# Optimization experiments

Measured on AMD Instinct MI355X. Metric: run time of the kernel, lower is better.

Reference implementation:

```python
import jax, jax.numpy as jnp
import numpy as np

B, K, D = 16384, 32, 64
N_USERS, N_ENT, N_REL = 100000, 100000, 32
MAX_NORM = 1.0


def renorm(e):
    # emulate torch nn.Embedding(max_norm=1): rescale rows with norm > 1
    n = jnp.linalg.norm(e, axis=-1, keepdims=True)
    return e * jnp.minimum(1.0, MAX_NORM / jnp.maximum(n, 1e-7))


def setup_inputs() -> dict:
    key = jax.random.key(0)
    ks = jax.random.split(key, 9)
    return {
        "user_table": jax.random.normal(ks[0], (N_USERS, D), dtype=jnp.float32),
        "entity_table": jax.random.normal(ks[1], (N_ENT, D), dtype=jnp.float32),
        "relation_table": jax.random.normal(ks[2], (N_REL, D), dtype=jnp.float32),
        "W": jax.random.normal(ks[3], (D, D), dtype=jnp.float32) / np.sqrt(D),
        "b": jnp.zeros((D,), dtype=jnp.float32),
        "users": jax.random.randint(ks[4], (B,), 0, N_USERS),
        "items": jax.random.randint(ks[5], (B,), 0, N_ENT),
        "adj_entity": jax.random.randint(ks[6], (N_ENT, K), 0, N_ENT),
        "adj_relation": jax.random.randint(ks[7], (N_ENT, K), 0, N_REL),
    }


def reference(user_table, entity_table, relation_table, W, b,
              users, items, adj_entity, adj_relation):
    # neighbor id gather: [B, K]
    nbr_ent_ids = adj_entity[items]
    nbr_rel_ids = adj_relation[items]
    # embedding lookups with max_norm renorm
    user_emb = renorm(user_table[users])                 # [B, D]
    item_emb = renorm(entity_table[items])               # [B, D]
    nbr_ent = renorm(entity_table[nbr_ent_ids])          # [B, K, D]
    nbr_rel = renorm(relation_table[nbr_rel_ids])        # [B, K, D]
    # user-relation attention scores, softmax over neighbors
    scores = jnp.einsum('bd,bkd->bk', user_emb, nbr_rel)  # [B, K]
    attn = jax.nn.softmax(scores, axis=-1)
    # attention-weighted neighbor aggregation
    nbr_vec = jnp.einsum('bk,bkd->bd', attn, nbr_ent)     # [B, D]
    # sum aggregator + linear + relu (dropout omitted: eval-mode baseline)
    out = item_emb + nbr_vec
    out = jax.nn.relu(out @ W.T + b)
    return (user_emb, out)
```

## Files before the change

### kernel.cpp

```cpp
#include <hip/hip_runtime.h>
#include <math.h>

#define BB 16384
#define KK_N 32
#define DD 64
#define N_ENT 100000
#define N_REL 32
#define NBLK 4096

__device__ __forceinline__ float dot4(float4 a, float4 b) {
    return a.x * b.x + a.y * b.y + a.z * b.z + a.w * b.w;
}

__global__ __launch_bounds__(256) void kgcn_fused(
    const float* __restrict__ user_table,
    const float* __restrict__ entity_table,
    const float* __restrict__ relation_table,
    const float* __restrict__ W,
    const float* __restrict__ bias,
    const int*   __restrict__ users,
    const int*   __restrict__ items,
    const int*   __restrict__ adj_entity,
    const int*   __restrict__ adj_relation,
    float* __restrict__ out_user,
    float* __restrict__ out_final)
{
    __shared__ __align__(16) float Wlds[64 * 64];
    __shared__ __align__(16) float RelLds[N_REL * DD];
    __shared__ __align__(16) float Vec[4][64];

    const int tid  = threadIdx.x;
    const int lane = tid & 63;
    const int wave = tid >> 6;
    const int grp  = lane >> 4;
    const int gl   = lane & 15;

    const int b = blockIdx.x * 4 + wave;
    const int uid = __builtin_amdgcn_readfirstlane(users[b]);
    const int iid = __builtin_amdgcn_readfirstlane(items[b]);

    const int kk = lane & 31;
    const int* abase = (lane < 32) ? adj_entity : adj_relation;
    const int adjv = abase[(size_t)iid * KK_N + kk];
    float4 uv = *reinterpret_cast<const float4*>(&user_table[(size_t)uid * DD + gl * 4]);
    float4 iv = *reinterpret_cast<const float4*>(&entity_table[(size_t)iid * DD + gl * 4]);

    #pragma unroll
    for (int it = 0; it < 4; ++it) {
        int i = tid + it * 256;
        float4 w4 = reinterpret_cast<const float4*>(W)[i];
        int d = i >> 4;
        int j = (i & 15) * 4;
        *reinterpret_cast<float4*>(&Wlds[d * 64 + (j ^ ((d & 15) << 2))]) = w4;
    }
    #pragma unroll
    for (int it = 0; it < 2; ++it) {
        int r = wave * 8 + it * 4 + grp;
        float4 v = reinterpret_cast<const float4*>(relation_table)[r * 16 + gl];
        float ss = dot4(v, v);
        #pragma unroll
        for (int m = 1; m < 16; m <<= 1) ss += __shfl_xor(ss, m, 64);
        float sc = fminf(1.0f, __builtin_amdgcn_rsqf(ss));
        v.x *= sc; v.y *= sc; v.z *= sc; v.w *= sc;
        *reinterpret_cast<float4*>(&RelLds[r * 64 + ((gl * 4) ^ ((r & 15) << 2))]) = v;
    }

    float ssu = dot4(uv, uv);
    #pragma unroll
    for (int m = 1; m < 16; m <<= 1) ssu += __shfl_xor(ssu, m, 64);
    float usc = fminf(1.0f, __builtin_amdgcn_rsqf(ssu));
    uv.x *= usc; uv.y *= usc; uv.z *= usc; uv.w *= usc;
    if (lane < 16)
        *reinterpret_cast<float4*>(&out_user[(size_t)b * DD + gl * 4]) = uv;

    int   eid[8];
    #pragma unroll
    for (int k0 = 0; k0 < 8; ++k0)
        eid[k0] = __shfl(adjv, k0 * 4 + grp, 64);
    float4 v[8];
    #pragma unroll
    for (int k0 = 0; k0 < 8; ++k0)
        v[k0] = *reinterpret_cast<const float4*>(&entity_table[(size_t)eid[k0] * DD + gl * 4]);

    __syncthreads();
    if (lane < 16)
        *reinterpret_cast<float4*>(&Vec[wave][gl * 4]) = uv;

    const int rid = __shfl(adjv, 32 + kk, 64);
    const int srel = (rid & 15) << 2;
    const float* relrow = &RelLds[rid * 64];
    const int dbase = (lane >> 5) * 32;
    float score = 0.0f;
    #pragma unroll
    for (int d0 = 0; d0 < 32; d0 += 4) {
        int d = dbase + d0;
        float4 rv = *reinterpret_cast<const float4*>(&relrow[d ^ srel]);
        float4 tv = *reinterpret_cast<const float4*>(&Vec[wave][d]);
        score += dot4(tv, rv);
    }
    score += __shfl_xor(score, 32, 64);

    float mx = score;
    #pragma unroll
    for (int m = 1; m < 32; m <<= 1) mx = fmaxf(mx, __shfl_xor(mx, m, 64));
    float e = __expf(score - mx);
    float sum = e;
    #pragma unroll
    for (int m = 1; m < 32; m <<= 1) sum += __shfl_xor(sum, m, 64);
    const float attn = e * __builtin_amdgcn_rcpf(sum);

    float cc[8];
    #pragma unroll
    for (int k0 = 0; k0 < 8; ++k0)
        cc[k0] = __shfl(attn, k0 * 4 + grp, 64);

    float4 acc = make_float4(0.f, 0.f, 0.f, 0.f);
    #pragma unroll
    for (int k0 = 0; k0 < 8; ++k0) {
        float ss = dot4(v[k0], v[k0]);
        #pragma unroll
        for (int m = 1; m < 16; m <<= 1) ss += __shfl_xor(ss, m, 64);
        float sc = fminf(1.0f, __builtin_amdgcn_rsqf(ss));
        float ck = cc[k0] * sc;
        acc.x = fmaf(ck, v[k0].x, acc.x);
        acc.y = fmaf(ck, v[k0].y, acc.y);
        acc.z = fmaf(ck, v[k0].z, acc.z);
        acc.w = fmaf(ck, v[k0].w, acc.w);
    }
    #pragma unroll
    for (int m = 16; m < 64; m <<= 1) {
        acc.x += __shfl_xor(acc.x, m, 64);
        acc.y += __shfl_xor(acc.y, m, 64);
        acc.z += __shfl_xor(acc.z, m, 64);
        acc.w += __shfl_xor(acc.w, m, 64);
    }

    float ssi = dot4(iv, iv);
    #pragma unroll
    for (int m = 1; m < 16; m <<= 1) ssi += __shfl_xor(ssi, m, 64);
    float isc = fminf(1.0f, __builtin_amdgcn_rsqf(ssi));
    float4 tmp;
    tmp.x = fmaf(isc, iv.x, acc.x);
    tmp.y = fmaf(isc, iv.y, acc.y);
    tmp.z = fmaf(isc, iv.z, acc.z);
    tmp.w = fmaf(isc, iv.w, acc.w);
    if (lane < 16)
        *reinterpret_cast<float4*>(&Vec[wave][gl * 4]) = tmp;

    const float bv = bias[lane];
    const float* wrow = &Wlds[lane * 64];
    const int twz = (lane & 15) << 2;
    float o = bv;
    #pragma unroll
    for (int j0 = 0; j0 < 64; j0 += 4) {
        float4 wv = *reinterpret_cast<const float4*>(&wrow[j0 ^ twz]);
        float4 tv = *reinterpret_cast<const float4*>(&Vec[wave][j0]);
        o += dot4(tv, wv);
    }
    out_final[(size_t)b * DD + lane] = fmaxf(o, 0.0f);
}

extern "C" void kernel_launch(void* const* d_in, const int* in_sizes, int n_in,
                              void* d_out, int out_size, void* d_ws, size_t ws_size,
                              hipStream_t stream)
{
    const float* user_table     = (const float*)d_in[0];
    const float* entity_table   = (const float*)d_in[1];
    const float* relation_table = (const float*)d_in[2];
    const float* W              = (const float*)d_in[3];
    const float* bias           = (const float*)d_in[4];
    const int*   users          = (const int*)d_in[5];
    const int*   items          = (const int*)d_in[6];
    const int*   adj_entity     = (const int*)d_in[7];
    const int*   adj_relation   = (const int*)d_in[8];

    float* out_user  = (float*)d_out;
    float* out_final = (float*)d_out + (size_t)BB * DD;

    kgcn_fused<<<NBLK, 256, 0, stream>>>(user_table, entity_table, relation_table,
                                         W, bias, users, items, adj_entity, adj_relation,
                                         out_user, out_final);
}
```

Baseline: 31.38 us.

## Precompute per-entity renorm scales in a separate pass before main kernel

Adds a precompute kernel that computes the max-norm scale for every entity row, writes the renormalized user rows straight to the output, and stores renormalized relation rows in workspace. The main kernel then reads these scales instead of redoing the per-neighbour norm reductions and shuffles, and loads the relation table from workspace. It also moves to 512-thread blocks handling 8 batch rows each. The cost is a full extra pass over the entity table plus a second kernel launch, which may outweigh the arithmetic and shuffle work removed from the gather-bound main kernel.

```diff
diff --git a/kernel.cpp b/kernel.cpp
--- a/kernel.cpp
+++ b/kernel.cpp
@@ -6,87 +6,117 @@
 #define DD 64
 #define N_ENT 100000
 #define N_REL 32
-#define NBLK 4096
+
+
+#define T_ENT  N_ENT
+#define T_USER (N_ENT + BB)
+#define T_ALL  (N_ENT + BB + N_REL)
 
 __device__ __forceinline__ float dot4(float4 a, float4 b) {
     return a.x * b.x + a.y * b.y + a.z * b.z + a.w * b.w;
 }
 
-__global__ __launch_bounds__(256) void kgcn_fused(
+__device__ __forceinline__ float red16(float ss) {
+    ss += __shfl_xor(ss, 1, 64);
+    ss += __shfl_xor(ss, 2, 64);
+    ss += __shfl_xor(ss, 4, 64);
+    ss += __shfl_xor(ss, 8, 64);
+    return ss;
+}
+
+__global__ __launch_bounds__(256) void precompute(
     const float* __restrict__ user_table,
     const float* __restrict__ entity_table,
     const float* __restrict__ relation_table,
+    const int*   __restrict__ users,
+    float* __restrict__ ws,
+    float* __restrict__ out_user)
+{
+    const int tid = threadIdx.x;
+    const int gl  = tid & 15;
+    const int t   = blockIdx.x * 16 + (tid >> 4);
+
+    if (t < T_ENT) {
+        float4 v = *reinterpret_cast<const float4*>(&entity_table[(size_t)t * DD + gl * 4]);
+        float ss = red16(dot4(v, v));
+        float sc = fminf(1.0f, __builtin_amdgcn_rsqf(ss));
+        if (gl == 0) ws[t] = sc;
+    } else if (t < T_USER) {
+        int u = t - T_ENT;
+        int uid = users[u];
+        float4 v = *reinterpret_cast<const float4*>(&user_table[(size_t)uid * DD + gl * 4]);
+        float ss = red16(dot4(v, v));
+        float sc = fminf(1.0f, __builtin_amdgcn_rsqf(ss));
+        v.x *= sc; v.y *= sc; v.z *= sc; v.w *= sc;
+        *reinterpret_cast<float4*>(&out_user[(size_t)u * DD + gl * 4]) = v;
+    } else if (t < T_ALL) {
+        int r = t - T_USER;
+        float4 v = *reinterpret_cast<const float4*>(&relation_table[r * DD + gl * 4]);
+        float ss = red16(dot4(v, v));
+        float sc = fminf(1.0f, __builtin_amdgcn_rsqf(ss));
+        v.x *= sc; v.y *= sc; v.z *= sc; v.w *= sc;
+        *reinterpret_cast<float4*>(&ws[N_ENT + r * 64 + ((gl * 4) ^ ((r & 15) << 2))]) = v;
+    }
+}
+
+__global__ __launch_bounds__(512, 8) void kgcn_main(
+    const float* __restrict__ entity_table,
+    const float* __restrict__ ws,
     const float* __restrict__ W,
     const float* __restrict__ bias,
-    const int*   __restrict__ users,
     const int*   __restrict__ items,
     const int*   __restrict__ adj_entity,
     const int*   __restrict__ adj_relation,
-    float* __restrict__ out_user,
+    const float* __restrict__ user_out,
     float* __restrict__ out_final)
 {
     __shared__ __align__(16) float Wlds[64 * 64];
     __shared__ __align__(16) float RelLds[N_REL * DD];
-    __shared__ __align__(16) float Vec[4][64];
+    __shared__ __align__(16) float Vec[8][64];
 
     const int tid  = threadIdx.x;
     const int lane = tid & 63;
     const int wave = tid >> 6;
     const int grp  = lane >> 4;
     const int gl   = lane & 15;
-
-    const int b = blockIdx.x * 4 + wave;
-    const int uid = __builtin_amdgcn_readfirstlane(users[b]);
+    const int kk   = lane & 31;
+
+    const int b = blockIdx.x * 8 + wave;
     const int iid = __builtin_amdgcn_readfirstlane(items[b]);
 
-    const int kk = lane & 31;
     const int* abase = (lane < 32) ? adj_entity : adj_relation;
     const int adjv = abase[(size_t)iid * KK_N + kk];
-    float4 uv = *reinterpret_cast<const float4*>(&user_table[(size_t)uid * DD + gl * 4]);
+    const float sg = ws[adjv];
+    const float isc = ws[iid];
+    float4 uv = *reinterpret_cast<const float4*>(&user_out[(size_t)b * DD + gl * 4]);
     float4 iv = *reinterpret_cast<const float4*>(&entity_table[(size_t)iid * DD + gl * 4]);
-
-    #pragma unroll
-    for (int it = 0; it < 4; ++it) {
-        int i = tid + it * 256;
+    const float bv = bias[lane];
+
+    int eid[8];
+    #pragma unroll
+    for (int k0 = 0; k0 < 8; ++k0)
+        eid[k0] = __shfl(adjv, k0 * 4 + grp, 64);
+    float4 v[8];
+    #pragma unroll
+    for (int k0 = 0; k0 < 8; ++k0)
+        v[k0] = *reinterpret_cast<const float4*>(&entity_table[(size_t)eid[k0] * DD + gl * 4]);
+
+    #pragma unroll
+    for (int it = 0; it < 2; ++it) {
+        int i = tid + it * 512;
         float4 w4 = reinterpret_cast<const float4*>(W)[i];
         int d = i >> 4;
         int j = (i & 15) * 4;
         *reinterpret_cast<float4*>(&Wlds[d * 64 + (j ^ ((d & 15) << 2))]) = w4;
     }
-    #pragma unroll
-    for (int it = 0; it < 2; ++it) {
-        int r = wave * 8 + it * 4 + grp;
-        float4 v = reinterpret_cast<const float4*>(relation_table)[r * 16 + gl];
-        float ss = dot4(v, v);
-        #pragma unroll
-        for (int m = 1; m < 16; m <<= 1) ss += __shfl_xor(ss, m, 64);
-        float sc = fminf(1.0f, __builtin_amdgcn_rsqf(ss));
-        v.x *= sc; v.y *= sc; v.z *= sc; v.w *= sc;
-        *reinterpret_cast<float4*>(&RelLds[r * 64 + ((gl * 4) ^ ((r & 15) << 2))]) = v;
-    }
-
-    float ssu = dot4(uv, uv);
-    #pragma unroll
-    for (int m = 1; m < 16; m <<= 1) ssu += __shfl_xor(ssu, m, 64);
-    float usc = fminf(1.0f, __builtin_amdgcn_rsqf(ssu));
-    uv.x *= usc; uv.y *= usc; uv.z *= usc; uv.w *= usc;
-    if (lane < 16)
-        *reinterpret_cast<float4*>(&out_user[(size_t)b * DD + gl * 4]) = uv;
-
-    int   eid[8];
-    #pragma unroll
-    for (int k0 = 0; k0 < 8; ++k0)
-        eid[k0] = __shfl(adjv, k0 * 4 + grp, 64);
-    float4 v[8];
-    #pragma unroll
-    for (int k0 = 0; k0 < 8; ++k0)
-        v[k0] = *reinterpret_cast<const float4*>(&entity_table[(size_t)eid[k0] * DD + gl * 4]);
+    reinterpret_cast<float4*>(RelLds)[tid] = reinterpret_cast<const float4*>(ws + N_ENT)[tid];
 
     __syncthreads();
+
     if (lane < 16)
         *reinterpret_cast<float4*>(&Vec[wave][gl * 4]) = uv;
 
-    const int rid = __shfl(adjv, 32 + kk, 64);
+    const int rid  = __shfl(adjv, 32 + kk, 64);
     const int srel = (rid & 15) << 2;
     const float* relrow = &RelLds[rid * 64];
     const int dbase = (lane >> 5) * 32;
@@ -107,21 +137,12 @@
     float sum = e;
     #pragma unroll
     for (int m = 1; m < 32; m <<= 1) sum += __shfl_xor(sum, m, 64);
-    const float attn = e * __builtin_amdgcn_rcpf(sum);
-
-    float cc[8];
-    #pragma unroll
-    for (int k0 = 0; k0 < 8; ++k0)
-        cc[k0] = __shfl(attn, k0 * 4 + grp, 64);
+    const float wk = e * __builtin_amdgcn_rcpf(sum) * sg;
 
     float4 acc = make_float4(0.f, 0.f, 0.f, 0.f);
     #pragma unroll
     for (int k0 = 0; k0 < 8; ++k0) {
-        float ss = dot4(v[k0], v[k0]);
-        #pragma unroll
-        for (int m = 1; m < 16; m <<= 1) ss += __shfl_xor(ss, m, 64);
-        float sc = fminf(1.0f, __builtin_amdgcn_rsqf(ss));
-        float ck = cc[k0] * sc;
+        float ck = __shfl(wk, k0 * 4 + grp, 64);
         acc.x = fmaf(ck, v[k0].x, acc.x);
         acc.y = fmaf(ck, v[k0].y, acc.y);
         acc.z = fmaf(ck, v[k0].z, acc.z);
@@ -135,10 +156,6 @@
         acc.w += __shfl_xor(acc.w, m, 64);
     }
 
-    float ssi = dot4(iv, iv);
-    #pragma unroll
-    for (int m = 1; m < 16; m <<= 1) ssi += __shfl_xor(ssi, m, 64);
-    float isc = fminf(1.0f, __builtin_amdgcn_rsqf(ssi));
     float4 tmp;
     tmp.x = fmaf(isc, iv.x, acc.x);
     tmp.y = fmaf(isc, iv.y, acc.y);
@@ -147,7 +164,6 @@
     if (lane < 16)
         *reinterpret_cast<float4*>(&Vec[wave][gl * 4]) = tmp;
 
-    const float bv = bias[lane];
     const float* wrow = &Wlds[lane * 64];
     const int twz = (lane & 15) << 2;
     float o = bv;
@@ -174,10 +190,13 @@
     const int*   adj_entity     = (const int*)d_in[7];
     const int*   adj_relation   = (const int*)d_in[8];
 
+    float* ws        = (float*)d_ws;
     float* out_user  = (float*)d_out;
     float* out_final = (float*)d_out + (size_t)BB * DD;
 
-    kgcn_fused<<<NBLK, 256, 0, stream>>>(user_table, entity_table, relation_table,
-                                         W, bias, users, items, adj_entity, adj_relation,
-                                         out_user, out_final);
-}
+    precompute<<<(T_ALL + 15) / 16, 256, 0, stream>>>(user_table, entity_table, relation_table,
+                                                      users, ws, out_user);
+    kgcn_main<<<BB / 8, 512, 0, stream>>>(entity_table, ws, W, bias,
+                                          items, adj_entity, adj_relation,
+                                          out_user, out_final);
+}
```

New measurement: 56.46 us. 79.9% more time.

## Precompute renormalized entity-times-W table and split into precompute and main kernels

Applied to the files above, without the earlier changes.

Because the final linear layer is linear, W is applied to every renormalized entity row in a precompute kernel, written to workspace. The main kernel then only gathers the transformed rows, mixes them with attention weights, adds bias and applies ReLU, with no per-sample 64x64 matvec. The precompute kernel also writes the renormalized user rows and a swizzled renormalized relation table. The softmax max-subtraction is dropped because all scores have magnitude at most 1 after renormalization. This trades per-sample W work and repeated renorms for a full pass over all 100k entities each call, plus the workspace write and a second launch.

```diff
diff --git a/kernel.cpp b/kernel.cpp
--- a/kernel.cpp
+++ b/kernel.cpp
@@ -6,10 +6,181 @@
 #define DD 64
 #define N_ENT 100000
 #define N_REL 32
-#define NBLK 4096
+
+#define NB_EW ((N_ENT + 63) / 64)
+#define NB_U  (BB / 16)
+#define NB_R  2
+#define GRID_PRE (NB_EW + NB_U + NB_R)
+
+#define WS_REL_OFF ((size_t)N_ENT * DD)
+#define WS_NEED_BYTES ((WS_REL_OFF + (size_t)N_REL * DD) * 4)
 
 __device__ __forceinline__ float dot4(float4 a, float4 b) {
     return a.x * b.x + a.y * b.y + a.z * b.z + a.w * b.w;
+}
+
+__device__ __forceinline__ float red16(float ss) {
+    ss += __shfl_xor(ss, 1, 64);
+    ss += __shfl_xor(ss, 2, 64);
+    ss += __shfl_xor(ss, 4, 64);
+    ss += __shfl_xor(ss, 8, 64);
+    return ss;
+}
+
+__global__ __launch_bounds__(256) void precompute(
+    const float* __restrict__ user_table,
+    const float* __restrict__ entity_table,
+    const float* __restrict__ relation_table,
+    const float* __restrict__ W,
+    const int*   __restrict__ users,
+    float* __restrict__ ws,
+    float* __restrict__ out_user)
+{
+    const int tid = threadIdx.x;
+    const int blk = blockIdx.x;
+
+    if (blk < NB_EW) {
+        const int lane = tid & 63;
+        const int row  = blk * 64 + lane;
+        const int d0   = __builtin_amdgcn_readfirstlane(tid >> 6) * 16;
+        const int r    = (row < N_ENT) ? row : 0;
+        const float* arow = entity_table + (size_t)r * DD;
+
+        float acc[16];
+        #pragma unroll
+        for (int i = 0; i < 16; ++i) acc[i] = 0.0f;
+        float ss = 0.0f;
+
+        #pragma unroll 1
+        for (int j0 = 0; j0 < DD; j0 += 4) {
+            float4 a = *reinterpret_cast<const float4*>(&arow[j0]);
+            ss += dot4(a, a);
+            #pragma unroll
+            for (int dd = 0; dd < 16; ++dd) {
+                float4 w = *reinterpret_cast<const float4*>(&W[(d0 + dd) * DD + j0]);
+                acc[dd] = fmaf(a.x, w.x, fmaf(a.y, w.y, fmaf(a.z, w.z, fmaf(a.w, w.w, acc[dd]))));
+            }
+        }
+        float sc = fminf(1.0f, __builtin_amdgcn_rsqf(ss));
+        if (row < N_ENT) {
+            #pragma unroll
+            for (int q = 0; q < 4; ++q) {
+                float4 o = make_float4(acc[q*4+0]*sc, acc[q*4+1]*sc, acc[q*4+2]*sc, acc[q*4+3]*sc);
+                *reinterpret_cast<float4*>(&ws[(size_t)row * DD + d0 + q * 4]) = o;
+            }
+        }
+    } else if (blk < NB_EW + NB_U) {
+        const int gl = tid & 15;
+        const int u  = (blk - NB_EW) * 16 + (tid >> 4);
+        const int uid = users[u];
+        float4 v = *reinterpret_cast<const float4*>(&user_table[(size_t)uid * DD + gl * 4]);
+        float ss = red16(dot4(v, v));
+        float sc = fminf(1.0f, __builtin_amdgcn_rsqf(ss));
+        v.x *= sc; v.y *= sc; v.z *= sc; v.w *= sc;
+        *reinterpret_cast<float4*>(&out_user[(size_t)u * DD + gl * 4]) = v;
+    } else {
+        const int gl = tid & 15;
+        const int rr = (blk - NB_EW - NB_U) * 16 + (tid >> 4);
+        float4 v = *reinterpret_cast<const float4*>(&relation_table[rr * DD + gl * 4]);
+        float ss = red16(dot4(v, v));
+        float sc = fminf(1.0f, __builtin_amdgcn_rsqf(ss));
+        v.x *= sc; v.y *= sc; v.z *= sc; v.w *= sc;
+        *reinterpret_cast<float4*>(&ws[WS_REL_OFF + rr * DD + ((gl * 4) ^ ((rr & 15) << 2))]) = v;
+    }
+}
+
+__global__ __launch_bounds__(256) void kgcn_main(
+    const float* __restrict__ ew,
+    const float* __restrict__ rel_ws,
+    const float* __restrict__ bias,
+    const int*   __restrict__ items,
+    const int*   __restrict__ adj_entity,
+    const int*   __restrict__ adj_relation,
+    const float* __restrict__ user_out,
+    float* __restrict__ out_final)
+{
+    __shared__ __align__(16) float RelLds[N_REL * DD];
+    __shared__ __align__(16) float Vec[4][64];
+
+    const int tid  = threadIdx.x;
+    const int lane = tid & 63;
+    const int wave = tid >> 6;
+    const int grp  = lane >> 4;
+    const int gl   = lane & 15;
+    const int kk   = lane & 31;
+
+    const int b = blockIdx.x * 4 + wave;
+    const int iid = __builtin_amdgcn_readfirstlane(items[b]);
+
+    const int* abase = (lane < 32) ? adj_entity : adj_relation;
+    const int adjv = abase[(size_t)iid * KK_N + kk];
+    float4 uv    = *reinterpret_cast<const float4*>(&user_out[(size_t)b * DD + gl * 4]);
+    float4 ewi   = *reinterpret_cast<const float4*>(&ew[(size_t)iid * DD + gl * 4]);
+    float4 bias4 = *reinterpret_cast<const float4*>(&bias[gl * 4]);
+
+    int eid[8];
+    #pragma unroll
+    for (int k0 = 0; k0 < 8; ++k0)
+        eid[k0] = adj_entity[(size_t)iid * KK_N + k0 * 4 + grp];
+    float4 v[8];
+    #pragma unroll
+    for (int k0 = 0; k0 < 8; ++k0)
+        v[k0] = *reinterpret_cast<const float4*>(&ew[(size_t)eid[k0] * DD + gl * 4]);
+
+    #pragma unroll
+    for (int it = 0; it < 2; ++it)
+        reinterpret_cast<float4*>(RelLds)[tid + it * 256] =
+            reinterpret_cast<const float4*>(rel_ws)[tid + it * 256];
+    __syncthreads();
+
+    if (lane < 16)
+        *reinterpret_cast<float4*>(&Vec[wave][gl * 4]) = uv;
+
+    const int rid  = __shfl(adjv, 32 + kk, 64);
+    const int srel = (rid & 15) << 2;
+    const float* relrow = &RelLds[rid * DD];
+    const int dbase = (lane >> 5) * 32;
+    float score = 0.0f;
+    #pragma unroll
+    for (int d0 = 0; d0 < 32; d0 += 4) {
+        int d = dbase + d0;
+        float4 rv = *reinterpret_cast<const float4*>(&relrow[d ^ srel]);
+        float4 tv = *reinterpret_cast<const float4*>(&Vec[wave][d]);
+        score += dot4(tv, rv);
+    }
+    score += __shfl_xor(score, 32, 64);
+
+    float e = __expf(score);
+    float sum = e;
+    #pragma unroll
+    for (int m = 1; m < 32; m <<= 1) sum += __shfl_xor(sum, m, 64);
+    const float wk = e * __builtin_amdgcn_rcpf(sum);
+
+    float4 acc = make_float4(0.f, 0.f, 0.f, 0.f);
+    #pragma unroll
+    for (int k0 = 0; k0 < 8; ++k0) {
+        float ck = __shfl(wk, k0 * 4 + grp, 64);
+        acc.x = fmaf(ck, v[k0].x, acc.x);
+        acc.y = fmaf(ck, v[k0].y, acc.y);
+        acc.z = fmaf(ck, v[k0].z, acc.z);
+        acc.w = fmaf(ck, v[k0].w, acc.w);
+    }
+    #pragma unroll
+    for (int m = 16; m < 64; m <<= 1) {
+        acc.x += __shfl_xor(acc.x, m, 64);
+        acc.y += __shfl_xor(acc.y, m, 64);
+        acc.z += __shfl_xor(acc.z, m, 64);
+        acc.w += __shfl_xor(acc.w, m, 64);
+    }
+
+    if (lane < 16) {
+        float4 o;
+        o.x = fmaxf(ewi.x + acc.x + bias4.x, 0.0f);
+        o.y = fmaxf(ewi.y + acc.y + bias4.y, 0.0f);
+        o.z = fmaxf(ewi.z + acc.z + bias4.z, 0.0f);
+        o.w = fmaxf(ewi.w + acc.w + bias4.w, 0.0f);
+        *reinterpret_cast<float4*>(&out_final[(size_t)b * DD + gl * 4]) = o;
+    }
 }
 
 __global__ __launch_bounds__(256) void kgcn_fused(
@@ -56,13 +227,13 @@
     #pragma unroll
     for (int it = 0; it < 2; ++it) {
         int r = wave * 8 + it * 4 + grp;
-        float4 v = reinterpret_cast<const float4*>(relation_table)[r * 16 + gl];
-        float ss = dot4(v, v);
+        float4 vv = reinterpret_cast<const float4*>(relation_table)[r * 16 + gl];
+        float ss = dot4(vv, vv);
         #pragma unroll
         for (int m = 1; m < 16; m <<= 1) ss += __shfl_xor(ss, m, 64);
         float sc = fminf(1.0f, __builtin_amdgcn_rsqf(ss));
-        v.x *= sc; v.y *= sc; v.z *= sc; v.w *= sc;
-        *reinterpret_cast<float4*>(&RelLds[r * 64 + ((gl * 4) ^ ((r & 15) << 2))]) = v;
+        vv.x *= sc; vv.y *= sc; vv.z *= sc; vv.w *= sc;
+        *reinterpret_cast<float4*>(&RelLds[r * 64 + ((gl * 4) ^ ((r & 15) << 2))]) = vv;
     }
 
     float ssu = dot4(uv, uv);
@@ -73,7 +244,7 @@
     if (lane < 16)
         *reinterpret_cast<float4*>(&out_user[(size_t)b * DD + gl * 4]) = uv;
 
-    int   eid[8];
+    int eid[8];
     #pragma unroll
     for (int k0 = 0; k0 < 8; ++k0)
         eid[k0] = __shfl(adjv, k0 * 4 + grp, 64);
@@ -174,10 +345,19 @@
     const int*   adj_entity     = (const int*)d_in[7];
     const int*   adj_relation   = (const int*)d_in[8];
 
+    float* ws        = (float*)d_ws;
     float* out_user  = (float*)d_out;
     float* out_final = (float*)d_out + (size_t)BB * DD;
 
-    kgcn_fused<<<NBLK, 256, 0, stream>>>(user_table, entity_table, relation_table,
-                                         W, bias, users, items, adj_entity, adj_relation,
-                                         out_user, out_final);
-}
+    if (ws_size >= WS_NEED_BYTES) {
+        precompute<<<GRID_PRE, 256, 0, stream>>>(user_table, entity_table, relation_table,
+                                                 W, users, ws, out_user);
+        kgcn_main<<<BB / 4, 256, 0, stream>>>(ws, ws + WS_REL_OFF, bias,
+                                              items, adj_entity, adj_relation,
+                                              out_user, out_final);
+    } else {
+        kgcn_fused<<<BB / 4, 256, 0, stream>>>(user_table, entity_table, relation_table,
+                                               W, bias, users, items, adj_entity, adj_relation,
+                                               out_user, out_final);
+    }
+}
```

Measured after the change: 51.70 us. 1.65x slower.

## Pre-renormalize entity table to bf16 in a workspace pass before main kernel

Applied to the files above, without the earlier changes.

A new precompute kernel renormalizes the whole entity table once per call and stores it as bf16 in the workspace. The same pass writes the renormalized user rows and a swizzled relation table. The main kernel then gathers half-width neighbor rows with no per-neighbor norm work, handles two batch rows per wave, and drops the softmax max subtraction because scores are bounded once rows are renormalized. This trades an extra full-table pass and a second launch for less gather traffic and ALU work, at the cost of bf16 rounding in the entity embeddings.

```diff
diff --git a/kernel.cpp b/kernel.cpp
--- a/kernel.cpp
+++ b/kernel.cpp
@@ -6,10 +6,226 @@
 #define DD 64
 #define N_ENT 100000
 #define N_REL 32
-#define NBLK 4096
+
+#define WS_REL_OFF_BYTES ((size_t)N_ENT * DD * 2)
+#define WS_NEED_BYTES (WS_REL_OFF_BYTES + (size_t)N_REL * DD * 4)
+
+#define PT_ENT  N_ENT
+#define PT_USER (N_ENT + BB)
+#define PT_ALL  (N_ENT + BB + N_REL)
 
 __device__ __forceinline__ float dot4(float4 a, float4 b) {
     return a.x * b.x + a.y * b.y + a.z * b.z + a.w * b.w;
+}
+
+__device__ __forceinline__ float red16(float ss) {
+    ss += __shfl_xor(ss, 1, 64);
+    ss += __shfl_xor(ss, 2, 64);
+    ss += __shfl_xor(ss, 4, 64);
+    ss += __shfl_xor(ss, 8, 64);
+    return ss;
+}
+
+__device__ __forceinline__ unsigned short f2bf(float x) {
+    unsigned int u = __float_as_uint(x);
+    u += 0x7fffu + ((u >> 16) & 1u);
+    return (unsigned short)(u >> 16);
+}
+
+__device__ __forceinline__ float bf2f(unsigned short h) {
+    return __uint_as_float(((unsigned int)h) << 16);
+}
+
+__device__ __forceinline__ float4 bf4(ushort4 h) {
+    return make_float4(bf2f(h.x), bf2f(h.y), bf2f(h.z), bf2f(h.w));
+}
+
+__global__ __launch_bounds__(256) void precompute(
+    const float* __restrict__ user_table,
+    const float* __restrict__ entity_table,
+    const float* __restrict__ relation_table,
+    const int*   __restrict__ users,
+    unsigned short* __restrict__ ent_bf,
+    float* __restrict__ rel_ws,
+    float* __restrict__ out_user)
+{
+    const int tid = threadIdx.x;
+    const int gl  = tid & 15;
+    const int t   = blockIdx.x * 16 + (tid >> 4);
+    if (t >= PT_ALL) return;
+
+    if (t < PT_ENT) {
+        float4 v = *reinterpret_cast<const float4*>(&entity_table[(size_t)t * DD + gl * 4]);
+        float ss = red16(dot4(v, v));
+        float sc = fminf(1.0f, __builtin_amdgcn_rsqf(ss));
+        ushort4 h;
+        h.x = f2bf(v.x * sc); h.y = f2bf(v.y * sc);
+        h.z = f2bf(v.z * sc); h.w = f2bf(v.w * sc);
+        *reinterpret_cast<ushort4*>(&ent_bf[(size_t)t * DD + gl * 4]) = h;
+    } else if (t < PT_USER) {
+        int u = t - PT_ENT;
+        int uid = users[u];
+        float4 v = *reinterpret_cast<const float4*>(&user_table[(size_t)uid * DD + gl * 4]);
+        float ss = red16(dot4(v, v));
+        float sc = fminf(1.0f, __builtin_amdgcn_rsqf(ss));
+        v.x *= sc; v.y *= sc; v.z *= sc; v.w *= sc;
+        *reinterpret_cast<float4*>(&out_user[(size_t)u * DD + gl * 4]) = v;
+    } else {
+        int rr = t - PT_USER;
+        float4 v = *reinterpret_cast<const float4*>(&relation_table[rr * DD + gl * 4]);
+        float ss = red16(dot4(v, v));
+        float sc = fminf(1.0f, __builtin_amdgcn_rsqf(ss));
+        v.x *= sc; v.y *= sc; v.z *= sc; v.w *= sc;
+        *reinterpret_cast<float4*>(&rel_ws[rr * DD + ((gl * 4) ^ ((rr & 15) << 2))]) = v;
+    }
+}
+
+__global__ __launch_bounds__(256, 4) void kgcn_main(
+    const unsigned short* __restrict__ ent_bf,
+    const float* __restrict__ rel_ws,
+    const float* __restrict__ W,
+    const float* __restrict__ bias,
+    const int*   __restrict__ items,
+    const int*   __restrict__ adj_entity,
+    const int*   __restrict__ adj_relation,
+    const float* __restrict__ user_out,
+    float* __restrict__ out_final)
+{
+    __shared__ __align__(16) float Wlds[64 * 64];
+    __shared__ __align__(16) float RelLds[N_REL * DD];
+    __shared__ __align__(16) float Vec[4][2][64];
+
+    const int tid  = threadIdx.x;
+    const int lane = tid & 63;
+    const int wave = tid >> 6;
+    const int grp  = lane >> 4;
+    const int gl   = lane & 15;
+    const int kk   = lane & 31;
+
+    const int b0 = (blockIdx.x * 4 + wave) * 2;
+    const int iid0 = __builtin_amdgcn_readfirstlane(items[b0]);
+    const int iid1 = __builtin_amdgcn_readfirstlane(items[b0 + 1]);
+
+    const int* abase = (lane < 32) ? adj_entity : adj_relation;
+    const int adjv0 = abase[(size_t)iid0 * KK_N + kk];
+    const int adjv1 = abase[(size_t)iid1 * KK_N + kk];
+
+    int eid0[8], eid1[8];
+    #pragma unroll
+    for (int k0 = 0; k0 < 8; ++k0) {
+        eid0[k0] = adj_entity[(size_t)iid0 * KK_N + k0 * 4 + grp];
+        eid1[k0] = adj_entity[(size_t)iid1 * KK_N + k0 * 4 + grp];
+    }
+    ushort4 v0[8], v1[8];
+    #pragma unroll
+    for (int k0 = 0; k0 < 8; ++k0) {
+        v0[k0] = *reinterpret_cast<const ushort4*>(&ent_bf[(size_t)eid0[k0] * DD + gl * 4]);
+        v1[k0] = *reinterpret_cast<const ushort4*>(&ent_bf[(size_t)eid1[k0] * DD + gl * 4]);
+    }
+    float4 uv0 = *reinterpret_cast<const float4*>(&user_out[(size_t)b0 * DD + gl * 4]);
+    float4 uv1 = *reinterpret_cast<const float4*>(&user_out[(size_t)(b0 + 1) * DD + gl * 4]);
+    ushort4 it0 = *reinterpret_cast<const ushort4*>(&ent_bf[(size_t)iid0 * DD + gl * 4]);
+    ushort4 it1 = *reinterpret_cast<const ushort4*>(&ent_bf[(size_t)iid1 * DD + gl * 4]);
+
+    #pragma unroll
+    for (int it = 0; it < 4; ++it) {
+        int i = tid + it * 256;
+        float4 w4 = reinterpret_cast<const float4*>(W)[i];
+        int d = i >> 4;
+        int j = (i & 15) * 4;
+        *reinterpret_cast<float4*>(&Wlds[d * 64 + (j ^ ((d & 15) << 2))]) = w4;
+    }
+    #pragma unroll
+    for (int it = 0; it < 2; ++it)
+        reinterpret_cast<float4*>(RelLds)[tid + it * 256] =
+            reinterpret_cast<const float4*>(rel_ws)[tid + it * 256];
+    __syncthreads();
+
+    if (lane < 16) {
+        *reinterpret_cast<float4*>(&Vec[wave][0][gl * 4]) = uv0;
+        *reinterpret_cast<float4*>(&Vec[wave][1][gl * 4]) = uv1;
+    }
+
+    const int rid0 = __shfl(adjv0, 32 + kk, 64);
+    const int rid1 = __shfl(adjv1, 32 + kk, 64);
+    const int sz0 = (rid0 & 15) << 2;
+    const int sz1 = (rid1 & 15) << 2;
+    const int dbase = (lane >> 5) * 32;
+    float s0 = 0.0f, s1 = 0.0f;
+    #pragma unroll
+    for (int d0 = 0; d0 < 32; d0 += 4) {
+        int d = dbase + d0;
+        float4 q0 = *reinterpret_cast<const float4*>(&Vec[wave][0][d]);
+        float4 r0 = *reinterpret_cast<const float4*>(&RelLds[rid0 * DD + (d ^ sz0)]);
+        s0 += dot4(q0, r0);
+        float4 q1 = *reinterpret_cast<const float4*>(&Vec[wave][1][d]);
+        float4 r1 = *reinterpret_cast<const float4*>(&RelLds[rid1 * DD + (d ^ sz1)]);
+        s1 += dot4(q1, r1);
+    }
+    s0 += __shfl_xor(s0, 32, 64);
+    s1 += __shfl_xor(s1, 32, 64);
+
+    float e0 = __expf(s0), e1 = __expf(s1);
+    float sum0 = e0, sum1 = e1;
+    #pragma unroll
+    for (int m = 1; m < 32; m <<= 1) {
+        sum0 += __shfl_xor(sum0, m, 64);
+        sum1 += __shfl_xor(sum1, m, 64);
+    }
+    const float wk0 = e0 * __builtin_amdgcn_rcpf(sum0);
+    const float wk1 = e1 * __builtin_amdgcn_rcpf(sum1);
+
+    float4 acc0 = make_float4(0.f, 0.f, 0.f, 0.f);
+    float4 acc1 = make_float4(0.f, 0.f, 0.f, 0.f);
+    #pragma unroll
+    for (int k0 = 0; k0 < 8; ++k0) {
+        float c0 = __shfl(wk0, k0 * 4 + grp, 64);
+        float4 f0 = bf4(v0[k0]);
+        acc0.x = fmaf(c0, f0.x, acc0.x);
+        acc0.y = fmaf(c0, f0.y, acc0.y);
+        acc0.z = fmaf(c0, f0.z, acc0.z);
+        acc0.w = fmaf(c0, f0.w, acc0.w);
+        float c1 = __shfl(wk1, k0 * 4 + grp, 64);
+        float4 f1 = bf4(v1[k0]);
+        acc1.x = fmaf(c1, f1.x, acc1.x);
+        acc1.y = fmaf(c1, f1.y, acc1.y);
+        acc1.z = fmaf(c1, f1.z, acc1.z);
+        acc1.w = fmaf(c1, f1.w, acc1.w);
+    }
+    #pragma unroll
+    for (int m = 16; m < 64; m <<= 1) {
+        acc0.x += __shfl_xor(acc0.x, m, 64);
+        acc0.y += __shfl_xor(acc0.y, m, 64);
+        acc0.z += __shfl_xor(acc0.z, m, 64);
+        acc0.w += __shfl_xor(acc0.w, m, 64);
+        acc1.x += __shfl_xor(acc1.x, m, 64);
+        acc1.y += __shfl_xor(acc1.y, m, 64);
+        acc1.z += __shfl_xor(acc1.z, m, 64);
+        acc1.w += __shfl_xor(acc1.w, m, 64);
+    }
+
+    float4 f0 = bf4(it0), f1 = bf4(it1);
+    float4 t0 = make_float4(f0.x + acc0.x, f0.y + acc0.y, f0.z + acc0.z, f0.w + acc0.w);
+    float4 t1 = make_float4(f1.x + acc1.x, f1.y + acc1.y, f1.z + acc1.z, f1.w + acc1.w);
+    if (lane < 16) {
+        *reinterpret_cast<float4*>(&Vec[wave][0][gl * 4]) = t0;
+        *reinterpret_cast<float4*>(&Vec[wave][1][gl * 4]) = t1;
+    }
+
+    const float bv = bias[lane];
+    const float* wrow = &Wlds[lane * 64];
+    const int twz = (lane & 15) << 2;
+    float o0 = bv, o1 = bv;
+    #pragma unroll
+    for (int j0 = 0; j0 < 64; j0 += 4) {
+        float4 wv = *reinterpret_cast<const float4*>(&wrow[j0 ^ twz]);
+        float4 q0 = *reinterpret_cast<const float4*>(&Vec[wave][0][j0]);
+        float4 q1 = *reinterpret_cast<const float4*>(&Vec[wave][1][j0]);
+        o0 += dot4(q0, wv);
+        o1 += dot4(q1, wv);
+    }
+    out_final[(size_t)b0 * DD + lane] = fmaxf(o0, 0.0f);
+    out_final[(size_t)(b0 + 1) * DD + lane] = fmaxf(o1, 0.0f);
 }
 
 __global__ __launch_bounds__(256) void kgcn_fused(
@@ -56,24 +272,20 @@
     #pragma unroll
     for (int it = 0; it < 2; ++it) {
         int r = wave * 8 + it * 4 + grp;
-        float4 v = reinterpret_cast<const float4*>(relation_table)[r * 16 + gl];
-        float ss = dot4(v, v);
-        #pragma unroll
-        for (int m = 1; m < 16; m <<= 1) ss += __shfl_xor(ss, m, 64);
+        float4 vv = reinterpret_cast<const float4*>(relation_table)[r * 16 + gl];
+        float ss = red16(dot4(vv, vv));
         float sc = fminf(1.0f, __builtin_amdgcn_rsqf(ss));
-        v.x *= sc; v.y *= sc; v.z *= sc; v.w *= sc;
-        *reinterpret_cast<float4*>(&RelLds[r * 64 + ((gl * 4) ^ ((r & 15) << 2))]) = v;
-    }
-
-    float ssu = dot4(uv, uv);
-    #pragma unroll
-    for (int m = 1; m < 16; m <<= 1) ssu += __shfl_xor(ssu, m, 64);
+        vv.x *= sc; vv.y *= sc; vv.z *= sc; vv.w *= sc;
+        *reinterpret_cast<float4*>(&RelLds[r * 64 + ((gl * 4) ^ ((r & 15) << 2))]) = vv;
+    }
+
+    float ssu = red16(dot4(uv, uv));
     float usc = fminf(1.0f, __builtin_amdgcn_rsqf(ssu));
     uv.x *= usc; uv.y *= usc; uv.z *= usc; uv.w *= usc;
     if (lane < 16)
         *reinterpret_cast<float4*>(&out_user[(size_t)b * DD + gl * 4]) = uv;
 
-    int   eid[8];
+    int eid[8];
     #pragma unroll
     for (int k0 = 0; k0 < 8; ++k0)
         eid[k0] = __shfl(adjv, k0 * 4 + grp, 64);
@@ -117,9 +329,7 @@
     float4 acc = make_float4(0.f, 0.f, 0.f, 0.f);
     #pragma unroll
     for (int k0 = 0; k0 < 8; ++k0) {
-        float ss = dot4(v[k0], v[k0]);
-        #pragma unroll
-        for (int m = 1; m < 16; m <<= 1) ss += __shfl_xor(ss, m, 64);
+        float ss = red16(dot4(v[k0], v[k0]));
         float sc = fminf(1.0f, __builtin_amdgcn_rsqf(ss));
         float ck = cc[k0] * sc;
         acc.x = fmaf(ck, v[k0].x, acc.x);
@@ -135,9 +345,7 @@
         acc.w += __shfl_xor(acc.w, m, 64);
     }
 
-    float ssi = dot4(iv, iv);
-    #pragma unroll
-    for (int m = 1; m < 16; m <<= 1) ssi += __shfl_xor(ssi, m, 64);
+    float ssi = red16(dot4(iv, iv));
     float isc = fminf(1.0f, __builtin_amdgcn_rsqf(ssi));
     float4 tmp;
     tmp.x = fmaf(isc, iv.x, acc.x);
@@ -177,7 +385,16 @@
     float* out_user  = (float*)d_out;
     float* out_final = (float*)d_out + (size_t)BB * DD;
 
-    kgcn_fused<<<NBLK, 256, 0, stream>>>(user_table, entity_table, relation_table,
-                                         W, bias, users, items, adj_entity, adj_relation,
-                                         out_user, out_final);
-}
+    if (ws_size >= WS_NEED_BYTES) {
+        unsigned short* ent_bf = (unsigned short*)d_ws;
+        float* rel_ws = (float*)((char*)d_ws + WS_REL_OFF_BYTES);
+        precompute<<<(PT_ALL + 15) / 16, 256, 0, stream>>>(
+            user_table, entity_table, relation_table, users, ent_bf, rel_ws, out_user);
+        kgcn_main<<<BB / 8, 256, 0, stream>>>(
+            ent_bf, rel_ws, W, bias, items, adj_entity, adj_relation, out_user, out_final);
+    } else {
+        kgcn_fused<<<BB / 4, 256, 0, stream>>>(user_table, entity_table, relation_table,
+                                               W, bias, users, items, adj_entity, adj_relation,
+                                               out_user, out_final);
+    }
+}
```

New measurement: 30.18 us (median of 3 runs). -3.8%, faster.
